# Optimization experiments

Measured on AMD Instinct MI355X. Metric: run time of the kernel, lower is better.

## Reference

```python
import jax, jax.numpy as jnp
import numpy as np

B = 32          # decode batch
H = 32          # query heads (TP shard)
KV_LORA = 512   # latent dim
ROPE = 64       # rope head dim
NOPE = 128      # nope head dim
VH = 128        # v head dim
QL = 1536       # q lora rank
HID = 5120      # model hidden
BLK = 128       # page/block size
BLOCKS_PER_SEQ = 32   # 4096-token context
NB = B * BLOCKS_PER_SEQ
CACHE_BLOCKS = 1200


def _rope(x, pos):
    # x: [B, n, ROPE] (neox half-rotation), pos: [B] int positions
    half = x.shape[-1] // 2
    inv = 1.0 / (10000.0 ** (jnp.arange(half, dtype=jnp.float32) / half))
    ang = pos.astype(jnp.float32)[:, None] * inv              # [B, half]
    cos, sin = jnp.cos(ang)[:, None, :], jnp.sin(ang)[:, None, :]
    x1, x2 = x[..., :half], x[..., half:]
    return jnp.concatenate([x1 * cos - x2 * sin, x2 * cos + x1 * sin], axis=-1)


def setup_inputs() -> dict:
    key = jax.random.key(0)
    ks = jax.random.split(key, 10)
    inp = {
        'hidden_states_or_q_c': jax.random.normal(ks[0], (B, QL), jnp.float32),
        'k_c_normed': jax.random.normal(ks[1], (B, 1, KV_LORA), jnp.float32),
        'k_pe': jax.random.normal(ks[2], (B, 1, ROPE), jnp.float32),
        'kv_cache_k': jax.random.normal(ks[3], (CACHE_BLOCKS, BLK, ROPE), jnp.float32),
        'kv_cache_v': jax.random.normal(ks[4], (CACHE_BLOCKS, BLK, KV_LORA), jnp.float32),
        'W_Q': jax.random.normal(ks[5], (QL, H * NOPE), jnp.float32) / np.sqrt(QL),
        'W_UK': jax.random.normal(ks[6], (H, NOPE, KV_LORA), jnp.float32) / np.sqrt(NOPE),
        'W_QR': jax.random.normal(ks[7], (QL, H * ROPE), jnp.float32) / np.sqrt(QL),
        'W_UV': jax.random.normal(ks[8], (H, KV_LORA, VH), jnp.float32) / np.sqrt(KV_LORA),
        'W_O': jax.random.normal(ks[9], (H * VH, HID), jnp.float32) / np.sqrt(H * VH),
        'input_positions': jnp.full((B,), BLK * BLOCKS_PER_SEQ - 1, jnp.int32),
        'block_list': jnp.arange(NB, dtype=jnp.int32),
        'block_groups': (jnp.arange(NB, dtype=jnp.int32) // BLOCKS_PER_SEQ),
        'block_bias': jnp.zeros((NB, BLK), jnp.float32),
        'block_indices': (jnp.arange(B, dtype=jnp.int32) * BLOCKS_PER_SEQ + BLOCKS_PER_SEQ - 1),
        'block_offsets': jnp.full((B,), BLK - 1, jnp.int32),
    }
    inp['block_mapping'] = jax.nn.one_hot(inp['block_groups'], B, dtype=jnp.float32)
    return inp


def reference(hidden_states_or_q_c, k_c_normed, k_pe, kv_cache_k, kv_cache_v,
              W_Q, W_UK, W_QR, W_UV, W_O,
              input_positions, block_list, block_groups, block_mapping,
              block_bias, block_indices, block_offsets):
    b = hidden_states_or_q_c.shape[0]
    h, nope, kv_lora = W_UK.shape
    rope = k_pe.shape[-1]
    scale = 1.0 / np.sqrt(nope + rope)

    # absorbed q projection: q_nope in latent space (_q_proj_and_k_up_proj)
    q_nope = jnp.einsum('bq,qhd->bhd', hidden_states_or_q_c, W_Q.reshape(-1, h, nope))
    q_nope = jnp.einsum('bhd,hdl->bhl', q_nope, W_UK)          # [B,H,kv_lora]
    q_pe = (hidden_states_or_q_c @ W_QR).reshape(b, h, rope)
    pos = input_positions.reshape(b)
    q_pe = _rope(q_pe, pos)
    k_pe_r = _rope(k_pe, pos)                                  # [B,1,rope]

    # write new latent token into paged cache (latent_cache_k / latent_cache_v)
    kv_cache_k = kv_cache_k.at[block_indices, block_offsets].set(k_pe_r[:, 0, :])
    kv_cache_v = kv_cache_v.at[block_indices, block_offsets].set(k_c_normed[:, 0, :])

    # flat_pa_mla: query [B,H,kv_lora+rope], key = concat(value_latent, k_pe)
    q = jnp.concatenate([q_nope, q_pe], axis=-1) * scale       # [B,H,576]
    keys = kv_cache_k[block_list]                              # [NB,BLK,rope]
    vals = kv_cache_v[block_list]                              # [NB,BLK,kv_lora]
    kcat = jnp.concatenate([vals, keys], axis=-1)              # [NB,BLK,576]

    qb = jnp.einsum('nb,bhd->nhd', block_mapping, q)           # batch2block
    logits = jnp.einsum('nhd,nkd->nhk', qb, kcat) + block_bias[:, None, :]

    # grouped (per-batch) softmax across this batch's blocks == pipelined_pa math
    gmax = jax.ops.segment_max(logits.max(-1), block_groups, num_segments=b)  # [B,H]
    p = jnp.exp(logits - gmax[block_groups][:, :, None])       # [NB,H,BLK]
    av = jnp.einsum('nhk,nkl->nhl', p, vals)                   # [NB,H,kv_lora]
    num = jnp.einsum('nb,nhl->bhl', block_mapping, av)         # block2batch
    den = jnp.einsum('nb,nh->bh', block_mapping, p.sum(-1))
    attn = num / den[..., None]                                # [B,H,kv_lora]

    # _v_up_proj_and_o_proj
    out = jnp.einsum('bhl,hlv->bhv', attn, W_UV).reshape(b, -1) @ W_O
    return out.reshape(b, 1, -1)
```

## Files before the change

### kernel.cpp

```cpp
#include <hip/hip_runtime.h>
#include <hip/hip_bf16.h>
#include <stdint.h>


typedef __attribute__((ext_vector_type(8))) short short8;
typedef __attribute__((ext_vector_type(4))) float f32x4;

__device__ inline uint32_t f2bf(float f) {
  uint32_t u = __float_as_uint(f);
  return (u + 0x7fffu + ((u >> 16) & 1u)) >> 16;
}
union Bf2U { __hip_bfloat162 h; uint32_t u; };
__device__ inline uint32_t pack2bf(float lo, float hi) {
  Bf2U v; v.h = __float22bfloat162_rn(float2{lo, hi});
  return v.u;
}
union FragU { uint32_t u[4]; short8 s; };
__device__ inline short8 frag_from(const uint32_t r[4]) {
  FragU v; v.u[0] = r[0]; v.u[1] = r[1]; v.u[2] = r[2]; v.u[3] = r[3];
  return v.s;
}

__global__ __launch_bounds__(256) void k1_qproj(
    const float* __restrict__ hidden, const float* __restrict__ W_Q,
    const float* __restrict__ W_QR, float* __restrict__ q_part) {
  __shared__ float hl[32][129];
  const int t = threadIdx.x;
  const int ctile = blockIdx.x * 128;
  const int k0 = blockIdx.y * 128;
  const bool isQ = (ctile < 4096);
  const float* W = isQ ? W_Q : W_QR;
  const int wstride = isQ ? 4096 : 2048;
  const int c = (isQ ? ctile : ctile - 4096) + (t & 31) * 4;
  const int gcol = ctile + (t & 31) * 4;
  const int rg = t >> 5;
  for (int idx = t; idx < 4096; idx += 256) {
    int b = idx >> 7, kk = idx & 127;
    hl[b][kk] = hidden[b * 1536 + k0 + kk];
  }
  __syncthreads();
  float acc[4][4];
#pragma unroll
  for (int r = 0; r < 4; ++r)
#pragma unroll
    for (int j = 0; j < 4; ++j) acc[r][j] = 0.f;
  const float* wp = W + (size_t)k0 * wstride + c;
#pragma unroll 4
  for (int kk = 0; kk < 128; ++kk) {
    float4 w = *(const float4*)wp;
    wp += wstride;
#pragma unroll
    for (int r = 0; r < 4; ++r) {
      float hv = hl[rg * 4 + r][kk];
      acc[r][0] += hv * w.x;
      acc[r][1] += hv * w.y;
      acc[r][2] += hv * w.z;
      acc[r][3] += hv * w.w;
    }
  }
  float* dst = q_part + (size_t)blockIdx.y * 32 * 6144;
#pragma unroll
  for (int r = 0; r < 4; ++r) {
    float4 v = make_float4(acc[r][0], acc[r][1], acc[r][2], acc[r][3]);
    *(float4*)&dst[(size_t)(rg * 4 + r) * 6144 + gcol] = v;
  }
}

__global__ __launch_bounds__(256) void k2_qlora(
    const float* __restrict__ q_part, const float* __restrict__ W_UK,
    float* __restrict__ q_acc2) {
  __shared__ float qn[32][33];
  const int t = threadIdx.x;
  const int h = blockIdx.y;
  const int c0 = blockIdx.x * 128;
  const int d0 = blockIdx.z * 32;
  for (int idx = t; idx < 1024; idx += 256) {
    int b = idx >> 5, dd = idx & 31;
    const int col = h * 128 + d0 + dd;
    float s = 0.f;
#pragma unroll
    for (int ks = 0; ks < 12; ++ks)
      s += q_part[(size_t)(ks * 32 + b) * 6144 + col];
    qn[b][dd] = s;
  }
  __syncthreads();
  const int c = c0 + (t & 31) * 4;
  const int rg = t >> 5;
  float acc[4][4];
#pragma unroll
  for (int r = 0; r < 4; ++r)
#pragma unroll
    for (int j = 0; j < 4; ++j) acc[r][j] = 0.f;
  const float* wp = W_UK + (size_t)(h * 128 + d0) * 512 + c;
#pragma unroll 4
  for (int dd = 0; dd < 32; ++dd) {
    float4 w = *(const float4*)wp;
    wp += 512;
#pragma unroll
    for (int r = 0; r < 4; ++r) {
      float qv = qn[rg * 4 + r][dd];
      acc[r][0] += qv * w.x;
      acc[r][1] += qv * w.y;
      acc[r][2] += qv * w.z;
      acc[r][3] += qv * w.w;
    }
  }
  const int ds = blockIdx.z;
  float* dst = q_acc2 + (size_t)ds * 524288;
#pragma unroll
  for (int r = 0; r < 4; ++r) {
    float4 v = make_float4(acc[r][0], acc[r][1], acc[r][2], acc[r][3]);
    *(float4*)&dst[(size_t)((rg * 4 + r) * 32 + h) * 512 + c] = v;
  }
}

__global__ __launch_bounds__(256) void k2b_rope_scatter(
    const float* __restrict__ q_part, const float* __restrict__ k_pe,
    const float* __restrict__ k_c_normed, const int* __restrict__ ipos,
    const int* __restrict__ bindices, const int* __restrict__ boffsets,
    const float* __restrict__ q_acc2, float* __restrict__ cache_k,
    float* __restrict__ cache_v, uint16_t* __restrict__ q_bf) {
  const int b = blockIdx.x;
  const int hs = blockIdx.y * 4;
  const int t = threadIdx.x;
  const float pos = (float)ipos[b];
  const float scale = 0.07216878364870323f;
  const float lnk = 0.28782313662425575f;
  for (int idx = t; idx < 2048; idx += 256) {
    int h = hs + (idx >> 9), c = idx & 511;
    const size_t base = (size_t)(b * 32 + h) * 512 + c;
    float s = q_acc2[base] + q_acc2[base + 524288] +
              q_acc2[base + 2 * 524288] + q_acc2[base + 3 * 524288];
    q_bf[((size_t)b * 32 + h) * 576 + c] = (uint16_t)f2bf(s * scale);
  }
  if (t < 128) {
    int h = hs + (t >> 5), i = t & 31;
    float ang = pos * __expf(-(float)i * lnk);
    float s, c;
    sincosf(ang, &s, &c);
    float x1 = 0.f, x2 = 0.f;
    const int col = 4096 + h * 64 + i;
#pragma unroll
    for (int ks = 0; ks < 12; ++ks) {
      const float* p = q_part + (size_t)(ks * 32 + b) * 6144 + col;
      x1 += p[0];
      x2 += p[32];
    }
    int base = (b * 32 + h) * 576 + 512;
    q_bf[base + i]      = (uint16_t)f2bf((x1 * c - x2 * s) * scale);
    q_bf[base + 32 + i] = (uint16_t)f2bf((x2 * c + x1 * s) * scale);
  }
  if (blockIdx.y == 0) {
    const int row = bindices[b] * 128 + boffsets[b];
    if (t < 32) {
      int i = t;
      float ang = pos * __expf(-(float)i * lnk);
      float s, c;
      sincosf(ang, &s, &c);
      float x1 = k_pe[b * 64 + i], x2 = k_pe[b * 64 + 32 + i];
      cache_k[row * 64 + i]      = x1 * c - x2 * s;
      cache_k[row * 64 + 32 + i] = x2 * c + x1 * s;
    }
    for (int j = t; j < 512; j += 256)
      cache_v[row * 512 + j] = k_c_normed[b * 512 + j];
  }
}

__global__ __launch_bounds__(256, 2) void k3_attn(
    const uint16_t* __restrict__ q_bf, const float* __restrict__ cache_k,
    const float* __restrict__ cache_v, const int* __restrict__ block_list,
    const int* __restrict__ block_groups, const float* __restrict__ block_bias,
    float* __restrict__ num_acc, float* __restrict__ den_acc) {
  __shared__ uint32_t Tl[288 * 33];
  __shared__ uint32_t Pl[16 * 33];
  __shared__ float den_sh[2][32];

  const int t = threadIdx.x;
  const int part = blockIdx.x, bseq = blockIdx.y;
  const int wave = t >> 6, lane = t & 63, quad = lane >> 4, l16 = lane & 15;
  const int hh = wave >> 1, kvh = wave & 1;
  const int n0 = bseq * 32 + part * 2;
  const int g = block_groups[n0];

  uint32_t qf[72];
  {
    const uint32_t* qrow =
        (const uint32_t*)(q_bf + (size_t)(g * 32 + hh * 16 + l16) * 576);
#pragma unroll
    for (int ks = 0; ks < 18; ++ks)
#pragma unroll
      for (int i = 0; i < 4; ++i)
        qf[ks * 4 + i] = qrow[ks * 16 + quad * 4 + i];
  }

  const f32x4 fzero = {0.f, 0.f, 0.f, 0.f};
  f32x4 acc[2][8];
#pragma unroll
  for (int mt = 0; mt < 2; ++mt)
#pragma unroll
    for (int nt = 0; nt < 8; ++nt) acc[mt][nt] = fzero;
  float den_acc_r[4] = {0.f, 0.f, 0.f, 0.f};

  for (int blk_i = 0; blk_i < 2; ++blk_i) {
    const int n = n0 + blk_i;
    const int phys = block_list[n];
    const float* vrow = cache_v + (size_t)phys * 128 * 512;
    const float* krow = cache_k + (size_t)phys * 128 * 64;
    for (int s = 0; s < 4; ++s) {
      const int s0 = s * 32;
      __syncthreads();
#pragma unroll
      for (int i = 0; i < 16; ++i) {
        int idx = i * 256 + t;
        int kv = idx >> 7, f4 = idx & 127;
        float4 v = *(const float4*)(vrow + (s0 + kv) * 512 + f4 * 4);
        int d2 = f4 * 2;
        Tl[(d2    ) * 33 + kv] = pack2bf(v.x, v.y);
        Tl[(d2 + 1) * 33 + kv] = pack2bf(v.z, v.w);
      }
#pragma unroll
      for (int i = 0; i < 2; ++i) {
        int idx = i * 256 + t;
        int kv = idx >> 4, f4 = idx & 15;
        float4 v = *(const float4*)(krow + (s0 + kv) * 64 + f4 * 4);
        int d2 = 256 + f4 * 2;
        Tl[(d2    ) * 33 + kv] = pack2bf(v.x, v.y);
        Tl[(d2 + 1) * 33 + kv] = pack2bf(v.z, v.w);
      }
      __syncthreads();
      const int tkv = kvh * 16 + l16;
      f32x4 lg = fzero;
#pragma unroll
      for (int ks = 0; ks < 18; ++ks) {
        uint32_t br[4];
#pragma unroll
        for (int i = 0; i < 4; ++i)
          br[i] = Tl[(ks * 16 + quad * 4 + i) * 33 + tkv];
        lg = __builtin_amdgcn_mfma_f32_16x16x32_bf16(
            frag_from(&qf[ks * 4]), frag_from(br), lg, 0, 0, 0);
      }
      float bias = block_bias[n * 128 + s0 + tkv];
      uint32_t pb[4];
#pragma unroll
      for (int r = 0; r < 4; ++r) {
        float p = __expf(lg[r] + bias);
        pb[r] = f2bf(p);
        den_acc_r[r] += __uint_as_float(pb[r] << 16);
      }
#pragma unroll
      for (int r = 0; r < 4; ++r) {
        uint32_t other = (uint32_t)__shfl_xor((int)pb[r], 1, 64);
        if ((l16 & 1) == 0) {
          int h = hh * 16 + quad * 4 + r;
          Pl[(tkv >> 1) * 33 + h] = pb[r] | (other << 16);
        }
      }
      __syncthreads();
      uint32_t af[2][4];
#pragma unroll
      for (int mt = 0; mt < 2; ++mt)
#pragma unroll
        for (int i = 0; i < 4; ++i)
          af[mt][i] = Pl[(quad * 4 + i) * 33 + mt * 16 + l16];
#pragma unroll
      for (int nt = 0; nt < 8; ++nt) {
        int l = wave * 128 + nt * 16 + l16;
        const uint32_t* base = &Tl[(l >> 1) * 33 + quad * 8];
        uint32_t dw[8];
#pragma unroll
        for (int j = 0; j < 8; ++j) dw[j] = base[j];
        uint32_t br[4];
        const bool odd = (l & 1);
#pragma unroll
        for (int i = 0; i < 4; ++i) {
          uint32_t a = dw[2 * i], bq = dw[2 * i + 1];
          uint32_t lo = odd ? (a >> 16) : (a & 0xffffu);
          uint32_t hi = odd ? (bq & 0xffff0000u) : (bq << 16);
          br[i] = lo | hi;
        }
        short8 bf = frag_from(br);
        acc[0][nt] = __builtin_amdgcn_mfma_f32_16x16x32_bf16(
            frag_from(af[0]), bf, acc[0][nt], 0, 0, 0);
        acc[1][nt] = __builtin_amdgcn_mfma_f32_16x16x32_bf16(
            frag_from(af[1]), bf, acc[1][nt], 0, 0, 0);
      }
    }
  }
#pragma unroll
  for (int mt = 0; mt < 2; ++mt)
#pragma unroll
    for (int nt = 0; nt < 8; ++nt)
#pragma unroll
      for (int r = 0; r < 4; ++r) {
        int h = mt * 16 + quad * 4 + r;
        int l = wave * 128 + nt * 16 + l16;
        atomicAdd(&num_acc[((size_t)(g * 32 + h)) * 512 + l], acc[mt][nt][r]);
      }
  float dv[4];
#pragma unroll
  for (int r = 0; r < 4; ++r) {
    float v = den_acc_r[r];
    v += __shfl_xor(v, 1, 64);
    v += __shfl_xor(v, 2, 64);
    v += __shfl_xor(v, 4, 64);
    v += __shfl_xor(v, 8, 64);
    dv[r] = v;
  }
  if (l16 == 0) {
#pragma unroll
    for (int r = 0; r < 4; ++r)
      den_sh[kvh][hh * 16 + quad * 4 + r] = dv[r];
  }
  __syncthreads();
  if (t < 32) atomicAdd(&den_acc[g * 32 + t], den_sh[0][t] + den_sh[1][t]);
}

__global__ __launch_bounds__(256) void k4_reduce_wuv(
    const float* __restrict__ num_acc, const float* __restrict__ den_acc,
    const float* __restrict__ W_UV, float* __restrict__ o_acc) {
  __shared__ float attn[32][65];
  __shared__ float inv[32];
  const int t = threadIdx.x;
  const int l0 = blockIdx.x * 64;
  const int h = blockIdx.y;
  if (t < 32) inv[t] = 1.f / den_acc[t * 32 + h];
  __syncthreads();
  for (int idx = t; idx < 2048; idx += 256) {
    int b = idx >> 6, l = idx & 63;
    attn[b][l] = num_acc[((size_t)(b * 32 + h)) * 512 + l0 + l] * inv[b];
  }
  __syncthreads();
  const int v = t & 127, rg = t >> 7;
  float acc[16];
#pragma unroll
  for (int r = 0; r < 16; ++r) acc[r] = 0.f;
  const float* wp = W_UV + ((size_t)h * 512 + l0) * 128 + v;
#pragma unroll 4
  for (int l = 0; l < 64; ++l) {
    float w = *wp;
    wp += 128;
#pragma unroll
    for (int r = 0; r < 16; ++r) acc[r] += attn[rg * 16 + r][l] * w;
  }
#pragma unroll
  for (int r = 0; r < 16; ++r)
    atomicAdd(&o_acc[(size_t)(rg * 16 + r) * 4096 + h * 128 + v], acc[r]);
}

__global__ __launch_bounds__(256) void k5_wo(
    const float* __restrict__ o_acc, const float* __restrict__ W_O,
    float* __restrict__ out) {
  __shared__ uint32_t Bt[32 * 130];
  const int t = threadIdx.x;
  const int ksplit = blockIdx.x, ntile = blockIdx.y;
  const int n0 = ntile * 128, kbase = ksplit * 256;
  const int wave = t >> 6, lane = t & 63, quad = lane >> 4, l16 = lane & 15;
  const f32x4 fzero = {0.f, 0.f, 0.f, 0.f};
  f32x4 acc[2][2];
#pragma unroll
  for (int mt = 0; mt < 2; ++mt)
#pragma unroll
    for (int nt = 0; nt < 2; ++nt) acc[mt][nt] = fzero;
  for (int kc = 0; kc < 4; ++kc) {
    const int k0 = kbase + kc * 64;
    __syncthreads();
    for (int idx = t; idx < 1024; idx += 256) {
      int k2 = idx >> 5, c4 = idx & 31;
      const float* p0 = &W_O[(size_t)(k0 + 2 * k2) * 5120 + n0 + c4 * 4];
      float4 a = *(const float4*)p0;
      float4 b = *(const float4*)(p0 + 5120);
      uint32_t* bp = &Bt[k2 * 130 + c4 * 4];
      bp[0] = pack2bf(a.x, b.x);
      bp[1] = pack2bf(a.y, b.y);
      bp[2] = pack2bf(a.z, b.z);
      bp[3] = pack2bf(a.w, b.w);
    }
    __syncthreads();
#pragma unroll
    for (int ks2 = 0; ks2 < 2; ++ks2) {
      uint32_t af[2][4];
#pragma unroll
      for (int mt = 0; mt < 2; ++mt) {
        const float* orow =
            o_acc + (size_t)(mt * 16 + l16) * 4096 + k0 + ks2 * 32 + quad * 8;
        float4 x = *(const float4*)orow;
        float4 y = *(const float4*)(orow + 4);
        af[mt][0] = pack2bf(x.x, x.y);
        af[mt][1] = pack2bf(x.z, x.w);
        af[mt][2] = pack2bf(y.x, y.y);
        af[mt][3] = pack2bf(y.z, y.w);
      }
#pragma unroll
      for (int nt = 0; nt < 2; ++nt) {
        uint32_t br[4];
#pragma unroll
        for (int i = 0; i < 4; ++i)
          br[i] = Bt[(ks2 * 16 + quad * 4 + i) * 130 + wave * 32 + nt * 16 + l16];
        short8 bf = frag_from(br);
        acc[0][nt] = __builtin_amdgcn_mfma_f32_16x16x32_bf16(
            frag_from(af[0]), bf, acc[0][nt], 0, 0, 0);
        acc[1][nt] = __builtin_amdgcn_mfma_f32_16x16x32_bf16(
            frag_from(af[1]), bf, acc[1][nt], 0, 0, 0);
      }
    }
  }
#pragma unroll
  for (int mt = 0; mt < 2; ++mt)
#pragma unroll
    for (int nt = 0; nt < 2; ++nt)
#pragma unroll
      for (int r = 0; r < 4; ++r) {
        int b = mt * 16 + quad * 4 + r;
        int c = n0 + wave * 32 + nt * 16 + l16;
        atomicAdd(&out[(size_t)b * 5120 + c], acc[mt][nt][r]);
      }
}

extern "C" void kernel_launch(void* const* d_in, const int* in_sizes, int n_in,
                              void* d_out, int out_size, void* d_ws,
                              size_t ws_size, hipStream_t stream) {
  (void)in_sizes; (void)n_in; (void)ws_size;
  const float* hidden = (const float*)d_in[0];
  const float* k_c    = (const float*)d_in[1];
  const float* k_pe   = (const float*)d_in[2];
  float* cache_k      = (float*)d_in[3];
  float* cache_v      = (float*)d_in[4];
  const float* W_Q    = (const float*)d_in[5];
  const float* W_UK   = (const float*)d_in[6];
  const float* W_QR   = (const float*)d_in[7];
  const float* W_UV   = (const float*)d_in[8];
  const float* W_O    = (const float*)d_in[9];
  const int* ipos     = (const int*)d_in[10];
  const int* blist    = (const int*)d_in[11];
  const int* bgroups  = (const int*)d_in[12];
  const float* bbias  = (const float*)d_in[13];
  const int* bindices = (const int*)d_in[14];
  const int* boffsets = (const int*)d_in[15];

  char* ws = (char*)d_ws;
  float*    o_acc    = (float*)(ws);
  float*    num_acc  = (float*)(ws + 524288);
  float*    den_acc  = (float*)(ws + 4718592);
  float*    q_part   = (float*)(ws + 4722688);
  float*    q_acc2   = (float*)(ws + 14159872);
  uint16_t* q_bf     = (uint16_t*)(ws + 22548480);
  float*    out      = (float*)d_out;

  hipMemsetAsync(ws, 0, 4722688, stream);
  hipMemsetAsync(d_out, 0, (size_t)out_size * sizeof(float), stream);

  k1_qproj<<<dim3(48, 12), 256, 0, stream>>>(hidden, W_Q, W_QR, q_part);
  k2_qlora<<<dim3(4, 32, 4), 256, 0, stream>>>(q_part, W_UK, q_acc2);
  k2b_rope_scatter<<<dim3(32, 8), 256, 0, stream>>>(q_part, k_pe, k_c, ipos,
                                                    bindices, boffsets, q_acc2,
                                                    cache_k, cache_v, q_bf);
  k3_attn<<<dim3(16, 32), 256, 0, stream>>>(q_bf, cache_k, cache_v, blist,
                                            bgroups, bbias, num_acc, den_acc);
  k4_reduce_wuv<<<dim3(8, 32), 256, 0, stream>>>(num_acc, den_acc, W_UV, o_acc);
  k5_wo<<<dim3(16, 40), 256, 0, stream>>>(o_acc, W_O, out);
}
```

Baseline: 648.0 us.

## Replace atomic accumulation with partial buffers and deterministic reduction kernels

The attention and output projection kernels now write per-split partial results to workspace instead of using float atomicAdd. The W_UV kernel reduces the 16 attention partials itself, and a new kernel sums the 16 K-split partials of the W_O GEMM. This removes the atomics and both memsets. In exchange it adds extra global traffic for the partials (about 32MB for num_part), one more launch, and a W_UV kernel with fewer blocks that each loop over the full 512-wide latent.

```diff
diff --git a/kernel.cpp b/kernel.cpp
--- a/kernel.cpp
+++ b/kernel.cpp
@@ -170,7 +170,7 @@
     const uint16_t* __restrict__ q_bf, const float* __restrict__ cache_k,
     const float* __restrict__ cache_v, const int* __restrict__ block_list,
     const int* __restrict__ block_groups, const float* __restrict__ block_bias,
-    float* __restrict__ num_acc, float* __restrict__ den_acc) {
+    float* __restrict__ num_part, float* __restrict__ den_part) {
   __shared__ uint32_t Tl[288 * 33];
   __shared__ uint32_t Pl[16 * 33];
   __shared__ float den_sh[2][32];
@@ -286,6 +286,7 @@
       }
     }
   }
+  float* npart = num_part + (size_t)(part * 32 + g) * 32 * 512;
 #pragma unroll
   for (int mt = 0; mt < 2; ++mt)
 #pragma unroll
@@ -294,7 +295,7 @@
       for (int r = 0; r < 4; ++r) {
         int h = mt * 16 + quad * 4 + r;
         int l = wave * 128 + nt * 16 + l16;
-        atomicAdd(&num_acc[((size_t)(g * 32 + h)) * 512 + l], acc[mt][nt][r]);
+        npart[(size_t)h * 512 + l] = acc[mt][nt][r];
       }
   float dv[4];
 #pragma unroll
@@ -312,44 +313,56 @@
       den_sh[kvh][hh * 16 + quad * 4 + r] = dv[r];
   }
   __syncthreads();
-  if (t < 32) atomicAdd(&den_acc[g * 32 + t], den_sh[0][t] + den_sh[1][t]);
+  if (t < 32)
+    den_part[(size_t)(part * 32 + g) * 32 + t] = den_sh[0][t] + den_sh[1][t];
 }
 
 __global__ __launch_bounds__(256) void k4_reduce_wuv(
-    const float* __restrict__ num_acc, const float* __restrict__ den_acc,
+    const float* __restrict__ num_part, const float* __restrict__ den_part,
     const float* __restrict__ W_UV, float* __restrict__ o_acc) {
-  __shared__ float attn[32][65];
-  __shared__ float inv[32];
-  const int t = threadIdx.x;
-  const int l0 = blockIdx.x * 64;
+  __shared__ float attn[8][516];
+  __shared__ float inv[8];
+  const int t = threadIdx.x;
+  const int bg = blockIdx.x;
   const int h = blockIdx.y;
-  if (t < 32) inv[t] = 1.f / den_acc[t * 32 + h];
+  if (t < 128) {
+    int b = t >> 4, p = t & 15;
+    float v = den_part[(size_t)(p * 32 + bg * 8 + b) * 32 + h];
+    v += __shfl_xor(v, 1, 64);
+    v += __shfl_xor(v, 2, 64);
+    v += __shfl_xor(v, 4, 64);
+    v += __shfl_xor(v, 8, 64);
+    if (p == 0) inv[b] = 1.f / v;
+  }
   __syncthreads();
-  for (int idx = t; idx < 2048; idx += 256) {
-    int b = idx >> 6, l = idx & 63;
-    attn[b][l] = num_acc[((size_t)(b * 32 + h)) * 512 + l0 + l] * inv[b];
+  for (int idx = t; idx < 4096; idx += 256) {
+    int b = idx >> 9, l = idx & 511;
+    const float* np =
+        num_part + ((size_t)(bg * 8 + b) * 32 + h) * 512 + l;
+    float s = 0.f;
+#pragma unroll
+    for (int p = 0; p < 16; ++p) s += np[(size_t)p * 524288];
+    attn[b][l] = s * inv[b];
   }
   __syncthreads();
   const int v = t & 127, rg = t >> 7;
-  float acc[16];
-#pragma unroll
-  for (int r = 0; r < 16; ++r) acc[r] = 0.f;
-  const float* wp = W_UV + ((size_t)h * 512 + l0) * 128 + v;
+  float acc[4] = {0.f, 0.f, 0.f, 0.f};
+  const float* wp = W_UV + (size_t)h * 512 * 128 + v;
 #pragma unroll 4
-  for (int l = 0; l < 64; ++l) {
+  for (int l = 0; l < 512; ++l) {
     float w = *wp;
     wp += 128;
 #pragma unroll
-    for (int r = 0; r < 16; ++r) acc[r] += attn[rg * 16 + r][l] * w;
-  }
-#pragma unroll
-  for (int r = 0; r < 16; ++r)
-    atomicAdd(&o_acc[(size_t)(rg * 16 + r) * 4096 + h * 128 + v], acc[r]);
+    for (int r = 0; r < 4; ++r) acc[r] += attn[rg * 4 + r][l] * w;
+  }
+#pragma unroll
+  for (int r = 0; r < 4; ++r)
+    o_acc[(size_t)(bg * 8 + rg * 4 + r) * 4096 + h * 128 + v] = acc[r];
 }
 
 __global__ __launch_bounds__(256) void k5_wo(
     const float* __restrict__ o_acc, const float* __restrict__ W_O,
-    float* __restrict__ out) {
+    float* __restrict__ out_part) {
   __shared__ uint32_t Bt[32 * 130];
   const int t = threadIdx.x;
   const int ksplit = blockIdx.x, ntile = blockIdx.y;
@@ -404,6 +417,7 @@
       }
     }
   }
+  float* dst = out_part + (size_t)ksplit * 32 * 5120;
 #pragma unroll
   for (int mt = 0; mt < 2; ++mt)
 #pragma unroll
@@ -412,14 +426,28 @@
       for (int r = 0; r < 4; ++r) {
         int b = mt * 16 + quad * 4 + r;
         int c = n0 + wave * 32 + nt * 16 + l16;
-        atomicAdd(&out[(size_t)b * 5120 + c], acc[mt][nt][r]);
-      }
+        dst[(size_t)b * 5120 + c] = acc[mt][nt][r];
+      }
+}
+
+__global__ __launch_bounds__(256) void k6_outsum(
+    const float* __restrict__ out_part, float* __restrict__ out) {
+  const int b = blockIdx.x;
+  const int c4 = blockIdx.y * 1024 + threadIdx.x * 4;
+  const float* p = out_part + (size_t)b * 5120 + c4;
+  float4 s = *(const float4*)p;
+#pragma unroll
+  for (int ks = 1; ks < 16; ++ks) {
+    float4 v = *(const float4*)(p + (size_t)ks * 163840);
+    s.x += v.x; s.y += v.y; s.z += v.z; s.w += v.w;
+  }
+  *(float4*)&out[(size_t)b * 5120 + c4] = s;
 }
 
 extern "C" void kernel_launch(void* const* d_in, const int* in_sizes, int n_in,
                               void* d_out, int out_size, void* d_ws,
                               size_t ws_size, hipStream_t stream) {
-  (void)in_sizes; (void)n_in; (void)ws_size;
+  (void)in_sizes; (void)n_in; (void)ws_size; (void)out_size;
   const float* hidden = (const float*)d_in[0];
   const float* k_c    = (const float*)d_in[1];
   const float* k_pe   = (const float*)d_in[2];
@@ -438,16 +466,14 @@
   const int* boffsets = (const int*)d_in[15];
 
   char* ws = (char*)d_ws;
-  float*    o_acc    = (float*)(ws);
-  float*    num_acc  = (float*)(ws + 524288);
-  float*    den_acc  = (float*)(ws + 4718592);
-  float*    q_part   = (float*)(ws + 4722688);
-  float*    q_acc2   = (float*)(ws + 14159872);
-  uint16_t* q_bf     = (uint16_t*)(ws + 22548480);
+  float*    q_part   = (float*)(ws);
+  float*    q_acc2   = (float*)(ws + 9437184);
+  uint16_t* q_bf     = (uint16_t*)(ws + 17825792);
+  float*    num_part = (float*)(ws + 19005440);
+  float*    den_part = (float*)(ws + 52559872);
+  float*    o_acc    = (float*)(ws + 52625408);
+  float*    out_part = (float*)(ws + 53149696);
   float*    out      = (float*)d_out;
-
-  hipMemsetAsync(ws, 0, 4722688, stream);
-  hipMemsetAsync(d_out, 0, (size_t)out_size * sizeof(float), stream);
 
   k1_qproj<<<dim3(48, 12), 256, 0, stream>>>(hidden, W_Q, W_QR, q_part);
   k2_qlora<<<dim3(4, 32, 4), 256, 0, stream>>>(q_part, W_UK, q_acc2);
@@ -455,7 +481,9 @@
                                                     bindices, boffsets, q_acc2,
                                                     cache_k, cache_v, q_bf);
   k3_attn<<<dim3(16, 32), 256, 0, stream>>>(q_bf, cache_k, cache_v, blist,
-                                            bgroups, bbias, num_acc, den_acc);
-  k4_reduce_wuv<<<dim3(8, 32), 256, 0, stream>>>(num_acc, den_acc, W_UV, o_acc);
-  k5_wo<<<dim3(16, 40), 256, 0, stream>>>(o_acc, W_O, out);
-}
+                                            bgroups, bbias, num_part, den_part);
+  k4_reduce_wuv<<<dim3(4, 32), 256, 0, stream>>>(num_part, den_part, W_UV,
+                                                 o_acc);
+  k5_wo<<<dim3(16, 40), 256, 0, stream>>>(o_acc, W_O, out_part);
+  k6_outsum<<<dim3(32, 5), 256, 0, stream>>>(out_part, out);
+}
```

Result: slower. 686.8 us (+6.0%).
